# Performance work log

Hardware: AMD Instinct MI355X
Metric: run time of the kernel (lower is better)

## Reference

```python
import jax, jax.numpy as jnp
import numpy as np

B, T, IMG = 64, 20, 64
IN_DIM = IMG * IMG          # 4096, from x.view(B,-1,64*64)
C_IN = 8                    # input_channels
R_DIM = C_IN * 1024         # 8192, reshape(B,20,-1,32,32) constraint
NF = 64                     # num_filters
Z_DIM = 256
LIN_IN = 2 * NF * 7 * 7     # 6272


def setup_inputs() -> dict:
    key = jax.random.key(0)
    ks = jax.random.split(key, 10)
    x = jax.random.normal(ks[0], (B, T, IMG, IMG), jnp.float32)
    Win = jax.random.normal(ks[1], (IN_DIM, R_DIM), jnp.float32) / np.sqrt(IN_DIM).astype(np.float32)
    U = jax.random.normal(ks[2], (IN_DIM, R_DIM), jnp.float32) / np.sqrt(IN_DIM).astype(np.float32)
    Wr = jax.random.normal(ks[3], (R_DIM, R_DIM), jnp.float32) / np.sqrt(R_DIM).astype(np.float32)
    conv1_w = jax.random.normal(ks[4], (NF, C_IN, 3, 3, 3), jnp.float32) * 0.05
    conv1_b = jax.random.normal(ks[5], (NF,), jnp.float32) * 0.01
    conv2_w = jax.random.normal(ks[6], (2 * NF, NF, 3, 4, 4), jnp.float32) * 0.05
    conv2_b = jax.random.normal(ks[7], (2 * NF,), jnp.float32) * 0.01
    lin_w = jax.random.normal(ks[8], (Z_DIM, LIN_IN), jnp.float32) * 0.02
    lin_b = jax.random.normal(ks[9], (Z_DIM,), jnp.float32) * 0.01
    return {"x": x, "Win": Win, "U": U, "Wr": Wr,
            "conv1_w": conv1_w, "conv1_b": conv1_b,
            "conv2_w": conv2_w, "conv2_b": conv2_b,
            "lin_w": lin_w, "lin_b": lin_b}


def reference(x, Win, U, Wr, conv1_w, conv1_b, conv2_w, conv2_b, lin_w, lin_b):
    Bn = x.shape[0]
    xf = x.reshape(Bn, T, IN_DIM)                      # (B,T,4096)
    h0 = jnp.tanh(xf[:, 0] @ Win)                      # (B,R)
    xU = jnp.einsum('bti,ir->tbr', xf[:, 1:], U)       # precompute input drive (T-1,B,R)

    def step(h, xu):
        h = jnp.tanh(xu + h @ Wr)
        return h, h

    _, hs = jax.lax.scan(step, h0, xU)                 # (T-1,B,R)
    H = jnp.concatenate([h0[None], hs], axis=0)        # (T,B,R)
    H = jnp.swapaxes(H, 0, 1)                          # (B,T,R)

    h = H.reshape(Bn, T, C_IN, 32, 32).transpose(0, 2, 1, 3, 4)  # (B,C,T,32,32)
    dn = ('NCDHW', 'OIDHW', 'NCDHW')
    y = jax.lax.conv_general_dilated(h, conv1_w, (1, 2, 2),
                                     [(1, 1), (1, 1), (1, 1)], dimension_numbers=dn)
    y = y + conv1_b[None, :, None, None, None]
    y = jax.nn.leaky_relu(y, 0.01)                     # (B,NF,20,16,16)
    y = jax.lax.conv_general_dilated(y, conv2_w, (1, 2, 2),
                                     [(1, 1), (0, 0), (0, 0)], dimension_numbers=dn)
    y = y + conv2_b[None, :, None, None, None]
    y = jax.nn.leaky_relu(y, 0.01)                     # (B,2NF,20,7,7)

    y = y.reshape(Bn, -1, T, LIN_IN)                   # (B,1,20,6272), same row-major view as torch
    y = y @ lin_w.T + lin_b                            # (B,1,20,Z_DIM)
    mu, log_var = jnp.split(y, 2, axis=3)
    return mu, log_var
```

## Files before the change

kernel.cpp:

```cpp
#include <hip/hip_runtime.h>

typedef __bf16 v8bf __attribute__((ext_vector_type(8)));
typedef float  v4f  __attribute__((ext_vector_type(4)));
typedef unsigned short us8 __attribute__((ext_vector_type(8)));

__device__ __forceinline__ float bf2f(unsigned short u) {
    union { unsigned int i; float f; } v; v.i = ((unsigned int)u) << 16; return v.f;
}
__device__ __forceinline__ unsigned short f2bf(float f) {
    union { float f; unsigned int i; } v; v.f = f;
    return (unsigned short)((v.i + 0x7fffu + ((v.i >> 16) & 1u)) >> 16);
}
__device__ __forceinline__ int sw(int b) { return b ^ (((b >> 7) & 7) << 4); }

__global__ __launch_bounds__(256)
void transpose_f32_bf16(const float* __restrict__ src,
                        unsigned short* __restrict__ dst, int K, int N)
{
    __shared__ unsigned short tile[64][72];
    const int tid = threadIdx.x;
    const int c0 = blockIdx.x * 64, r0 = blockIdx.y * 64;
    const int tr = tid >> 2, tc4 = tid & 3;
    const float* sp = src + (size_t)(r0 + tr) * N + c0 + tc4 * 16;
#pragma unroll
    for (int j = 0; j < 4; ++j) {
        v4f f = *reinterpret_cast<const v4f*>(sp + j * 4);
#pragma unroll
        for (int e = 0; e < 4; ++e) tile[tr][tc4 * 16 + j * 4 + e] = f2bf(f[e]);
    }
    __syncthreads();
    const int ow = tid >> 3, och = tid & 7;
#pragma unroll
    for (int p = 0; p < 2; ++p) {
        int orow = p * 32 + ow;
        us8 o;
#pragma unroll
        for (int e = 0; e < 8; ++e) o[e] = tile[och * 8 + e][orow];
        *reinterpret_cast<us8*>(dst + (size_t)(c0 + orow) * K + r0 + och * 8) = o;
    }
}

__global__ __launch_bounds__(256)
void transpose_f32_bf16_tiled(const float* __restrict__ src,
                              unsigned short* __restrict__ dst, int N, int ktiles)
{
    __shared__ unsigned short tile[64][72];
    const int tid = threadIdx.x;
    const int c0 = blockIdx.x * 64, r0 = blockIdx.y * 64;
    const int tr = tid >> 2, tc4 = tid & 3;
    const float* sp = src + (size_t)(r0 + tr) * N + c0 + tc4 * 16;
#pragma unroll
    for (int j = 0; j < 4; ++j) {
        v4f f = *reinterpret_cast<const v4f*>(sp + j * 4);
#pragma unroll
        for (int e = 0; e < 4; ++e) tile[tr][tc4 * 16 + j * 4 + e] = f2bf(f[e]);
    }
    __syncthreads();
    const int ow = tid >> 3, och = tid & 7;
    unsigned short* tb = dst + ((size_t)blockIdx.x * ktiles + blockIdx.y) * 4096;
#pragma unroll
    for (int p = 0; p < 2; ++p) {
        int orow = p * 32 + ow;
        us8 o;
#pragma unroll
        for (int e = 0; e < 8; ++e) o[e] = tile[och * 8 + e][orow];
        *reinterpret_cast<us8*>(tb + orow * 64 + (och ^ (orow & 7)) * 8) = o;
    }
}

__global__ __launch_bounds__(256)
void cvt_x(const float* __restrict__ x, unsigned short* __restrict__ xb)
{
    int i = blockIdx.x * 256 + threadIdx.x;
    if (i >= 655360) return;
    v4f f0 = *reinterpret_cast<const v4f*>(x + (size_t)i * 8);
    v4f f1 = *reinterpret_cast<const v4f*>(x + (size_t)i * 8 + 4);
    us8 o;
#pragma unroll
    for (int e = 0; e < 4; ++e) { o[e] = f2bf(f0[e]); o[4 + e] = f2bf(f1[e]); }
    *reinterpret_cast<us8*>(xb + (size_t)i * 8) = o;
}

template<int BN, bool STORE_BF16, bool AF32, bool BF32, bool SWAPXY>
__global__ __launch_bounds__(256, 2)
void gemm_bt(const void* __restrict__ Ap, int lda_lo, int lda_hi,
             const void* __restrict__ BTp, int ldb,
             void* __restrict__ Cout, int ldc,
             int ksub, long long csplit_stride)
{
    constexpr int FN  = BN / 32;
    constexpr int BCH = BN / 32;
    const int tid = threadIdx.x;
    const int lane = tid & 63, wid = tid >> 6;
    const int wr = wid >> 1, wc = wid & 1;
    const int nt = SWAPXY ? blockIdx.y : blockIdx.x;
    const int mt = SWAPXY ? blockIdx.x : blockIdx.y;
    const int kz = blockIdx.z;
    const int n0 = nt * BN;
    const int kstart = kz * ksub;

    __shared__ unsigned short smem[(64 + BN) * 64];
    char* As = reinterpret_cast<char*>(smem);
    char* Bs = reinterpret_cast<char*>(smem + 64 * 64);

    const unsigned short* A16 = (const unsigned short*)Ap;
    const float*          A32 = (const float*)Ap;
    const unsigned short* B16 = (const unsigned short*)BTp;
    const float*          B32 = (const float*)BTp;

    const int arow = AF32 ? (tid >> 2) : (tid >> 3);
    const int aq   = AF32 ? (tid & 3) : (tid & 7);
    const float* Ab32 = A32 + (size_t)arow * lda_lo + (size_t)mt * lda_hi + kstart + aq * 16;
    const unsigned short* Ab16 = A16 + (size_t)arow * lda_lo + (size_t)mt * lda_hi + kstart + aq * 8;
    const int brow = tid >> 3, bq = tid & 7;
    const float* Bb32 = B32 + (size_t)(n0 + brow) * ldb + kstart + bq * 8;
    const unsigned short* Bb16 = B16 + (size_t)(n0 + brow) * ldb + kstart + bq * 8;

    v4f fa[4];
    us8 ra[2];
    v4f fb[BCH][2];
    us8 rb[BCH];

    auto load = [&](int kk) {
        if (AF32) {
#pragma unroll
            for (int j = 0; j < 4; ++j)
                fa[j] = *reinterpret_cast<const v4f*>(Ab32 + kk + j * 4);
        } else {
#pragma unroll
            for (int p = 0; p < 2; ++p)
                ra[p] = *reinterpret_cast<const us8*>(Ab16 + (size_t)(p * 32) * lda_lo + kk);
        }
        if (BF32) {
#pragma unroll
            for (int p = 0; p < BCH; ++p) {
                fb[p][0] = *reinterpret_cast<const v4f*>(Bb32 + (size_t)(p * 32) * ldb + kk);
                fb[p][1] = *reinterpret_cast<const v4f*>(Bb32 + (size_t)(p * 32) * ldb + kk + 4);
            }
        } else {
#pragma unroll
            for (int p = 0; p < BCH; ++p)
                rb[p] = *reinterpret_cast<const us8*>(Bb16 + (size_t)(p * 32) * ldb + kk);
        }
    };
    auto stage = [&]() {
        if (AF32) {
#pragma unroll
            for (int h = 0; h < 2; ++h) {
                us8 v;
#pragma unroll
                for (int e = 0; e < 8; ++e) v[e] = f2bf(fa[h * 2 + (e >> 2)][e & 3]);
                *reinterpret_cast<us8*>(As + arow * 128 + (((aq * 2 + h) * 16) ^ ((arow & 7) << 4))) = v;
            }
        } else {
#pragma unroll
            for (int p = 0; p < 2; ++p)
                *reinterpret_cast<us8*>(As + (arow + p * 32) * 128 + ((aq * 16) ^ ((arow & 7) << 4))) = ra[p];
        }
#pragma unroll
        for (int p = 0; p < BCH; ++p) {
            us8 v;
            if (BF32) {
#pragma unroll
                for (int e = 0; e < 8; ++e) v[e] = f2bf(fb[p][e >> 2][e & 3]);
            } else v = rb[p];
            *reinterpret_cast<us8*>(Bs + (brow + p * 32) * 128 + ((bq * 16) ^ ((brow & 7) << 4))) = v;
        }
    };

    v4f z4 = {0.f, 0.f, 0.f, 0.f};
    v4f acc[2][FN];
#pragma unroll
    for (int i = 0; i < 2; ++i)
#pragma unroll
        for (int j = 0; j < FN; ++j) acc[i][j] = z4;

    const int l15 = lane & 15, l4 = lane >> 4;
    const int nk = ksub / 64;
    load(0);
    for (int it = 0; it < nk; ++it) {
        __syncthreads();
        stage();
        __syncthreads();
        if (it + 1 < nk) load((it + 1) * 64);
#pragma unroll
        for (int ks = 0; ks < 2; ++ks) {
            const int kb = (ks * 32 + l4 * 8) * 2;
            v8bf af[2], bfr[FN];
#pragma unroll
            for (int fm = 0; fm < 2; ++fm) {
                int row = wr * 32 + fm * 16 + l15;
                af[fm] = *reinterpret_cast<const v8bf*>(As + row * 128 + (kb ^ ((row & 7) << 4)));
            }
#pragma unroll
            for (int fn = 0; fn < FN; ++fn) {
                int row = wc * (BN / 2) + fn * 16 + l15;
                bfr[fn] = *reinterpret_cast<const v8bf*>(Bs + row * 128 + (kb ^ ((row & 7) << 4)));
            }
#pragma unroll
            for (int fm = 0; fm < 2; ++fm)
#pragma unroll
                for (int fn = 0; fn < FN; ++fn)
                    acc[fm][fn] = __builtin_amdgcn_mfma_f32_16x16x32_bf16(af[fm], bfr[fn], acc[fm][fn], 0, 0, 0);
        }
    }
    const long long m0 = (long long)mt * 64;
#pragma unroll
    for (int fm = 0; fm < 2; ++fm)
#pragma unroll
        for (int fn = 0; fn < FN; ++fn)
#pragma unroll
            for (int r = 0; r < 4; ++r) {
                long long row = m0 + wr * 32 + fm * 16 + l4 * 4 + r;
                long long col = n0 + wc * (BN / 2) + fn * 16 + l15;
                long long idx = (long long)kz * csplit_stride + row * ldc + col;
                if (STORE_BF16) reinterpret_cast<unsigned short*>(Cout)[idx] = f2bf(acc[fm][fn][r]);
                else            reinterpret_cast<float*>(Cout)[idx]          = acc[fm][fn][r];
            }
}

#define KZ 4
__global__ __launch_bounds__(256, 2)
void scan_step(const unsigned short* __restrict__ A, int lda,
               const unsigned short* __restrict__ BTiles, int ktiles,
               int kper,
               const unsigned short* __restrict__ xu,
               unsigned short* __restrict__ hnext,
               unsigned short* __restrict__ Hbf, int t,
               float* __restrict__ part,
               unsigned int* __restrict__ tickets)
{
    const int tid = threadIdx.x, lane = tid & 63, wid = tid >> 6;
    const int wr = wid >> 1, wc = wid & 1;
    const int nt = blockIdx.x & 127, kz = blockIdx.x >> 7;
    const int n0 = nt * 64, kstart = kz * kper;
    const int l15 = lane & 15, l4 = lane >> 4;
    const int nit = kper >> 6;

    __shared__ unsigned short smem[32768];
    char* base = reinterpret_cast<char*>(smem);

    const int srow = tid >> 3, sq = tid & 7;
    const int gslot = sq ^ (srow & 7);
    const unsigned short* Asrc = A + (size_t)srow * lda + kstart + gslot * 8;
    const unsigned short* Bsrc = BTiles
        + ((size_t)(nt * ktiles + kz * (kper >> 6))) * 4096 + tid * 8;

    auto stage = [&](int buf, int it) {
        char* dA = base + buf * 16384 + wid * 1024;
        char* dB = dA + 8192;
        const int kk = it * 64;
#pragma unroll
        for (int p = 0; p < 2; ++p) {
            __builtin_amdgcn_global_load_lds(
                (const __attribute__((address_space(1))) void*)(Asrc + kk + (size_t)p * 32 * lda),
                (__attribute__((address_space(3))) void*)(dA + p * 4096), 16, 0, 0);
            __builtin_amdgcn_global_load_lds(
                (const __attribute__((address_space(1))) void*)(Bsrc + (size_t)it * 4096 + p * 2048),
                (__attribute__((address_space(3))) void*)(dB + p * 4096), 16, 0, 0);
        }
    };

    v4f acc00 = {0.f, 0.f, 0.f, 0.f};
    v4f acc01 = acc00, acc10 = acc00, acc11 = acc00;

    stage(0, 0); stage(1, 1); stage(2, 2);
    for (int it = 0; it < nit; ++it) {
        const int ahead = nit - 1 - it;
        if (ahead >= 2)      asm volatile("s_waitcnt vmcnt(8)" ::: "memory");
        else if (ahead == 1) asm volatile("s_waitcnt vmcnt(4)" ::: "memory");
        else                 asm volatile("s_waitcnt vmcnt(0)" ::: "memory");
        __builtin_amdgcn_s_barrier();
        __builtin_amdgcn_sched_barrier(0);
        if (it + 3 < nit) stage((it + 3) & 3, it + 3);
        const char* As = base + (it & 3) * 16384;
        const char* Bs = As + 8192;
#pragma unroll
        for (int ks = 0; ks < 2; ++ks) {
            const int kb = (ks * 32 + l4 * 8) * 2;
            v8bf a0, a1, b0, b1;
            { int row = wr * 32 + l15;      a0 = *reinterpret_cast<const v8bf*>(As + row * 128 + (kb ^ ((row & 7) << 4))); }
            { int row = wr * 32 + 16 + l15; a1 = *reinterpret_cast<const v8bf*>(As + row * 128 + (kb ^ ((row & 7) << 4))); }
            { int row = wc * 32 + l15;      b0 = *reinterpret_cast<const v8bf*>(Bs + row * 128 + (kb ^ ((row & 7) << 4))); }
            { int row = wc * 32 + 16 + l15; b1 = *reinterpret_cast<const v8bf*>(Bs + row * 128 + (kb ^ ((row & 7) << 4))); }
            acc00 = __builtin_amdgcn_mfma_f32_16x16x32_bf16(a0, b0, acc00, 0, 0, 0);
            acc01 = __builtin_amdgcn_mfma_f32_16x16x32_bf16(a0, b1, acc01, 0, 0, 0);
            acc10 = __builtin_amdgcn_mfma_f32_16x16x32_bf16(a1, b0, acc10, 0, 0, 0);
            acc11 = __builtin_amdgcn_mfma_f32_16x16x32_bf16(a1, b1, acc11, 0, 0, 0);
        }
    }

    float* mypart = part + (size_t)kz * 524288;
#pragma unroll
    for (int r = 0; r < 4; ++r) {
        int row0 = wr * 32 + l4 * 4 + r;
        int col0 = n0 + wc * 32 + l15;
        mypart[(size_t)row0 * 8192 + col0]             = acc00[r];
        mypart[(size_t)row0 * 8192 + col0 + 16]        = acc01[r];
        mypart[(size_t)(row0 + 16) * 8192 + col0]      = acc10[r];
        mypart[(size_t)(row0 + 16) * 8192 + col0 + 16] = acc11[r];
    }

    __shared__ int lastflag;
    __syncthreads();
    if (tid == 0) {
        unsigned int old = __hip_atomic_fetch_add(&tickets[nt], 1u,
                              __ATOMIC_ACQ_REL, __HIP_MEMORY_SCOPE_AGENT);
        lastflag = (old == KZ - 1);
    }
    __syncthreads();
    if (!lastflag) return;

    const int row = tid >> 2;
    const int c0 = n0 + (tid & 3) * 16;
    float pre[16];
    if (xu) {
        const us8* xp = reinterpret_cast<const us8*>(xu + (size_t)row * 8192 + c0);
        us8 x0 = xp[0], x1 = xp[1];
#pragma unroll
        for (int j = 0; j < 8; ++j) { pre[j] = bf2f(x0[j]); pre[8 + j] = bf2f(x1[j]); }
    } else {
#pragma unroll
        for (int j = 0; j < 16; ++j) pre[j] = 0.f;
    }
#pragma unroll
    for (int z = 0; z < KZ; ++z) {
        const float* pp = part + (size_t)z * 524288 + (size_t)row * 8192 + c0;
#pragma unroll
        for (int q = 0; q < 4; ++q) {
            v4f v = *reinterpret_cast<const v4f*>(pp + q * 4);
#pragma unroll
            for (int e = 0; e < 4; ++e) pre[q * 4 + e] += v[e];
        }
    }
    us8 o0, o1;
#pragma unroll
    for (int j = 0; j < 16; ++j) {
        unsigned short hb = f2bf(tanhf(pre[j]));
        if (j < 8) o0[j] = hb; else o1[j - 8] = hb;
        int col = c0 + j;
        Hbf[(((size_t)row * 20 + t) * 1024 + (col & 1023)) * 8 + (col >> 10)] = hb;
    }
    *reinterpret_cast<us8*>(hnext + (size_t)row * 8192 + c0)     = o0;
    *reinterpret_cast<us8*>(hnext + (size_t)row * 8192 + c0 + 8) = o1;
    if (tid == 0)
        __hip_atomic_store(&tickets[nt], 0u, __ATOMIC_RELAXED, __HIP_MEMORY_SCOPE_AGENT);
}

__global__ __launch_bounds__(256)
void cvt_w1(const float* __restrict__ w, unsigned short* __restrict__ o,
            unsigned int* __restrict__ tickets)
{
    if (blockIdx.x == 0 && threadIdx.x < 128) tickets[threadIdx.x] = 0;
    int idx = blockIdx.x * 256 + threadIdx.x;
    if (idx >= 64 * 224) return;
    int co = idx / 224, k = idx % 224;
    int g = k >> 3, ci = k & 7;
    float v = 0.f;
    if (g < 27) {
        int dt = g / 9, rr = g % 9, dy = rr / 3, dx = rr % 3;
        v = w[(((co * 8 + ci) * 3 + dt) * 3 + dy) * 3 + dx];
    }
    o[idx] = f2bf(v);
}
__global__ __launch_bounds__(256)
void cvt_w2(const float* __restrict__ w, unsigned short* __restrict__ o)
{
    int idx = blockIdx.x * 256 + threadIdx.x;
    if (idx >= 128 * 3072) return;
    int co = idx / 3072, k = idx % 3072;
    int g = k >> 6, ci = k & 63;
    int dt = g >> 4, dy = (g >> 2) & 3, dx = g & 3;
    o[idx] = f2bf(w[(((co * 64 + ci) * 3 + dt) * 4 + dy) * 4 + dx]);
}

__global__ __launch_bounds__(256, 2)
void conv1_kernel(const unsigned short* __restrict__ H,
                  const unsigned short* __restrict__ w1,
                  const float* __restrict__ bias,
                  unsigned short* __restrict__ y1)
{
    const int b = blockIdx.x, t = blockIdx.y;
    const int tid = threadIdx.x, lane = tid & 63, wid = tid >> 6;
    __shared__ unsigned short in_s[3 * 33 * 33 * 8];
    __shared__ unsigned short w_s[64 * 224];

    for (int i = tid; i < 13068; i += 256) reinterpret_cast<unsigned int*>(in_s)[i] = 0;
    __syncthreads();
    for (int idx = tid; idx < 3 * 1024; idx += 256) {
        int dt = idx >> 10, rem = idx & 1023;
        int iy = rem >> 5, ix = rem & 31;
        int ts = t + dt - 1;
        if (ts >= 0 && ts < 20) {
            us8 v = *reinterpret_cast<const us8*>(H + (((size_t)b * 20 + ts) * 1024 + rem) * 8);
            int byte = ((dt * 33 + iy + 1) * 33 + (ix + 1)) * 16;
            *reinterpret_cast<us8*>(reinterpret_cast<char*>(in_s) + sw(byte)) = v;
        }
    }
    for (int idx = tid; idx < 64 * 28; idx += 256) {
        int co = idx / 28, j = idx % 28;
        us8 v = *reinterpret_cast<const us8*>(w1 + co * 224 + j * 8);
        *reinterpret_cast<us8*>(reinterpret_cast<char*>(w_s) + sw(co * 448 + j * 16)) = v;
    }
    __syncthreads();

    const int l15 = lane & 15, l4 = lane >> 4;
    const int m_lo = wid * 64 + l15;
    v4f z4 = {0.f, 0.f, 0.f, 0.f};
    v4f acc[4][4];
#pragma unroll
    for (int i = 0; i < 4; ++i)
#pragma unroll
        for (int j = 0; j < 4; ++j) acc[i][j] = z4;

#pragma unroll
    for (int ks = 0; ks < 7; ++ks) {
        int g = ks * 4 + l4;
        int gc = g < 27 ? g : 26;
        int dt = gc / 9, rr = gc % 9, dy = rr / 3, dx = rr % 3;
        v8bf ap[4], aw[4];
#pragma unroll
        for (int fm = 0; fm < 4; ++fm) {
            int m = fm * 16 + m_lo;
            int py = m >> 4, px = m & 15;
            int byte = ((dt * 33 + 2 * py + dy) * 33 + 2 * px + dx) * 16;
            ap[fm] = *reinterpret_cast<const v8bf*>(reinterpret_cast<const char*>(in_s) + sw(byte));
        }
        int kb2 = (ks * 32 + l4 * 8) * 2;
#pragma unroll
        for (int fc = 0; fc < 4; ++fc) {
            int co = fc * 16 + l15;
            aw[fc] = *reinterpret_cast<const v8bf*>(reinterpret_cast<const char*>(w_s) + sw(co * 448 + kb2));
        }
#pragma unroll
        for (int fm = 0; fm < 4; ++fm)
#pragma unroll
            for (int fc = 0; fc < 4; ++fc)
                acc[fm][fc] = __builtin_amdgcn_mfma_f32_16x16x32_bf16(ap[fm], aw[fc], acc[fm][fc], 0, 0, 0);
    }
#pragma unroll
    for (int fm = 0; fm < 4; ++fm)
#pragma unroll
        for (int fc = 0; fc < 4; ++fc)
#pragma unroll
            for (int r = 0; r < 4; ++r) {
                int m  = wid * 64 + fm * 16 + l4 * 4 + r;
                int co = fc * 16 + l15;
                float v = acc[fm][fc][r] + bias[co];
                v = v > 0.f ? v : 0.01f * v;
                y1[(((size_t)b * 20 + t) * 256 + m) * 64 + co] = f2bf(v);
            }
}

__global__ __launch_bounds__(512, 2)
void conv2_kernel(const unsigned short* __restrict__ y1,
                  const unsigned short* __restrict__ w2,
                  const float* __restrict__ bias,
                  unsigned short* __restrict__ y2)
{
    const int b = blockIdx.x, t = blockIdx.y;
    const int tid = threadIdx.x, lane = tid & 63, wid = tid >> 6;
    const int wc = wid >> 1, wr = wid & 1;
    __shared__ unsigned short in_s[256 * 64];
    __shared__ unsigned short w_s[128 * 128];
    const int l15 = lane & 15, l4 = lane >> 4;

    const int m0v = wr * 32 + l15, m1v = m0v + 16;
    const int m0c = m0v < 49 ? m0v : 48, m1c = m1v < 49 ? m1v : 48;
    const int py0 = m0c / 7, px0 = m0c - py0 * 7;
    const int py1 = m1c / 7, px1 = m1c - py1 * 7;

    v4f acc[2][2];
#pragma unroll
    for (int i = 0; i < 2; ++i)
#pragma unroll
        for (int j = 0; j < 2; ++j) acc[i][j] = (v4f){0.f, 0.f, 0.f, 0.f};

    for (int dt = 0; dt < 3; ++dt) {
        int ts = t + dt - 1;
        __syncthreads();
        if (ts < 0 || ts >= 20) continue;
#pragma unroll
        for (int p = 0; p < 4; ++p) {
            int idx = tid + p * 512;
            int slot = idx >> 3, c8 = idx & 7;
            int yy = slot >> 4, xx = slot & 15;
            us8 v = *reinterpret_cast<const us8*>(y1 + (((size_t)b * 20 + ts) * 256 + slot) * 64 + c8 * 8);
            int cell = ((yy & 1) * 2 + (xx & 1)) * 64 + (yy >> 1) * 8 + (xx >> 1);
            int byte = cell * 128 + ((c8 * 16) ^ (((cell ^ (cell >> 3)) & 7) << 4));
            *reinterpret_cast<us8*>(reinterpret_cast<char*>(in_s) + byte) = v;
        }
        for (int kc = 0; kc < 8; ++kc) {
            __syncthreads();
#pragma unroll
            for (int p = 0; p < 4; ++p) {
                int idx = tid + p * 512;
                int co = idx >> 4, j = idx & 15;
                us8 v = *reinterpret_cast<const us8*>(w2 + (size_t)co * 3072 + dt * 1024 + kc * 128 + j * 8);
                *reinterpret_cast<us8*>(reinterpret_cast<char*>(w_s) + co * 256 + ((j * 16) ^ ((co & 7) << 4))) = v;
            }
            __syncthreads();
#pragma unroll
            for (int ks = 0; ks < 4; ++ks) {
                int klocal = ks * 32 + l4 * 8;
                int kk = kc * 128 + klocal;
                int dy = (kk >> 8) & 3, dx = (kk >> 6) & 3, ci0 = kk & 63;
                v8bf aw[2], bp[2];
#pragma unroll
                for (int fc = 0; fc < 2; ++fc) {
                    int co = wc * 32 + fc * 16 + l15;
                    aw[fc] = *reinterpret_cast<const v8bf*>(reinterpret_cast<const char*>(w_s)
                               + co * 256 + ((klocal * 2) ^ ((co & 7) << 4)));
                }
                int plane = ((dy & 1) << 1) | (dx & 1);
                int c0 = plane * 64 + (py0 + (dy >> 1)) * 8 + px0 + (dx >> 1);
                int c1 = plane * 64 + (py1 + (dy >> 1)) * 8 + px1 + (dx >> 1);
                bp[0] = *reinterpret_cast<const v8bf*>(reinterpret_cast<const char*>(in_s)
                          + c0 * 128 + ((ci0 * 2) ^ (((c0 ^ (c0 >> 3)) & 7) << 4)));
                bp[1] = *reinterpret_cast<const v8bf*>(reinterpret_cast<const char*>(in_s)
                          + c1 * 128 + ((ci0 * 2) ^ (((c1 ^ (c1 >> 3)) & 7) << 4)));
#pragma unroll
                for (int fc = 0; fc < 2; ++fc)
#pragma unroll
                    for (int fm = 0; fm < 2; ++fm)
                        acc[fc][fm] = __builtin_amdgcn_mfma_f32_16x16x32_bf16(aw[fc], bp[fm], acc[fc][fm], 0, 0, 0);
            }
        }
    }
#pragma unroll
    for (int fc = 0; fc < 2; ++fc)
#pragma unroll
        for (int fm = 0; fm < 2; ++fm)
#pragma unroll
            for (int r = 0; r < 4; ++r) {
                int co = wc * 32 + fc * 16 + l4 * 4 + r;
                int m  = wr * 32 + fm * 16 + l15;
                if (m < 49) {
                    float v = acc[fc][fm][r] + bias[co];
                    v = v > 0.f ? v : 0.01f * v;
                    y2[(((size_t)b * 128 + co) * 20 + t) * 49 + m] = f2bf(v);
                }
            }
}

__global__ __launch_bounds__(256)
void lin_epi(const float* __restrict__ linC, const float* __restrict__ lb,
             float* __restrict__ out)
{
    int i = blockIdx.x * 256 + threadIdx.x;
    int m = i >> 8, n = i & 255;
    float v = lb[n];
#pragma unroll
    for (int z = 0; z < 7; ++z) v += linC[(size_t)z * 327680 + i];
    size_t o = (n < 128) ? ((size_t)m * 128 + n) : (163840 + (size_t)m * 128 + (n - 128));
    out[o] = v;
}

extern "C" void kernel_launch(void* const* d_in, const int* in_sizes, int n_in,
                              void* d_out, int out_size, void* d_ws, size_t ws_size,
                              hipStream_t stream)
{
    const float* x   = (const float*)d_in[0];
    const float* Win = (const float*)d_in[1];
    const float* U   = (const float*)d_in[2];
    const float* Wr  = (const float*)d_in[3];
    const float* c1w = (const float*)d_in[4];
    const float* c1b = (const float*)d_in[5];
    const float* c2w = (const float*)d_in[6];
    const float* c2b = (const float*)d_in[7];
    const float* lw  = (const float*)d_in[8];
    const float* lb  = (const float*)d_in[9];

    char* ws = (char*)d_ws;
    unsigned short* WrTile = (unsigned short*)(ws);
    unsigned short* xbf  = (unsigned short*)(ws);
    unsigned short* WT   = (unsigned short*)(ws + 134217728ll);
    unsigned short* y1   = (unsigned short*)(ws + 134217728ll);
    unsigned short* y2   = (unsigned short*)(ws + 176160768ll);
    unsigned short* XALL = (unsigned short*)(ws + 201326592ll);
    unsigned short* Hbf  = (unsigned short*)(ws + 222298112ll);
    unsigned short* hb0  = (unsigned short*)(ws + 243269632ll);
    unsigned short* hb1  = (unsigned short*)(ws + 244318208ll);
    float*          part = (float*)        (ws + 245366784ll);
    float*          linC = (float*)        (ws + 245366784ll);
    unsigned short* w1bf = (unsigned short*)(ws + 254541824ll);
    unsigned short* w2bf = (unsigned short*)(ws + 254570496ll);
    unsigned int*   tick = (unsigned int*) (ws + 255356928ll);
    float*          out  = (float*)d_out;

    cvt_w1<<<56, 256, 0, stream>>>(c1w, w1bf, tick);
    cvt_w2<<<1536, 256, 0, stream>>>(c2w, w2bf);
    cvt_x<<<2560, 256, 0, stream>>>(x, xbf);

    transpose_f32_bf16_tiled<<<dim3(128, 64), 256, 0, stream>>>(Win, WT, 8192, 64);
    scan_step<<<512, 256, 0, stream>>>(xbf, 81920, WT, 64, 1024,
                                       (const unsigned short*)nullptr, hb0, Hbf, 0, part, tick);

    transpose_f32_bf16<<<dim3(128, 64), 256, 0, stream>>>(U, WT, 4096, 8192);
    gemm_bt<128, true, true, false, true><<<dim3(19, 64, 1), 256, 0, stream>>>(
        x + 4096, 81920, 4096, WT, 4096, XALL + 524288, 8192, 4096, 0ll);

    transpose_f32_bf16_tiled<<<dim3(128, 128), 256, 0, stream>>>(Wr, WrTile, 8192, 128);
    for (int t = 1; t < 20; ++t) {
        const unsigned short* hprev = (t & 1) ? hb0 : hb1;
        unsigned short*       hnext = (t & 1) ? hb1 : hb0;
        scan_step<<<512, 256, 0, stream>>>(hprev, 8192, WrTile, 128, 2048,
                                           XALL + (size_t)t * 524288, hnext, Hbf, t, part, tick);
    }

    conv1_kernel<<<dim3(64, 20), 256, 0, stream>>>(Hbf, w1bf, c1b, y1);
    conv2_kernel<<<dim3(64, 20), 512, 0, stream>>>(y1, w2bf, c2b, y2);

    gemm_bt<128, false, false, true, false><<<dim3(2, 20, 7), 256, 0, stream>>>(
        y2, 6272, 6272 * 64, lw, 6272, linC, 256, 896, 327680ll);
    lin_epi<<<1280, 256, 0, stream>>>(linC, lb, out);
}
```

Before: 1.549 ms.

## Add 8-way split-K scan step with 64x64 tiles and async LDS loads

New measurement: 1.811 ms. +16.9%, slower.

```diff
diff --git a/kernel.cpp b/kernel.cpp
--- a/kernel.cpp
+++ b/kernel.cpp
@@ -81,7 +81,7 @@
     *reinterpret_cast<us8*>(xb + (size_t)i * 8) = o;
 }
 
-template<int BN, bool STORE_BF16, bool AF32, bool BF32, bool SWAPXY>
+template<int BN, bool STORE_BF16, bool AF32, bool BF32>
 __global__ __launch_bounds__(256, 2)
 void gemm_bt(const void* __restrict__ Ap, int lda_lo, int lda_hi,
              const void* __restrict__ BTp, int ldb,
@@ -93,9 +93,7 @@
     const int tid = threadIdx.x;
     const int lane = tid & 63, wid = tid >> 6;
     const int wr = wid >> 1, wc = wid & 1;
-    const int nt = SWAPXY ? blockIdx.y : blockIdx.x;
-    const int mt = SWAPXY ? blockIdx.x : blockIdx.y;
-    const int kz = blockIdx.z;
+    const int nt = blockIdx.x, mt = blockIdx.y, kz = blockIdx.z;
     const int n0 = nt * BN;
     const int kstart = kz * ksub;
 
@@ -325,6 +323,134 @@
     }
 #pragma unroll
     for (int z = 0; z < KZ; ++z) {
+        const float* pp = part + (size_t)z * 524288 + (size_t)row * 8192 + c0;
+#pragma unroll
+        for (int q = 0; q < 4; ++q) {
+            v4f v = *reinterpret_cast<const v4f*>(pp + q * 4);
+#pragma unroll
+            for (int e = 0; e < 4; ++e) pre[q * 4 + e] += v[e];
+        }
+    }
+    us8 o0, o1;
+#pragma unroll
+    for (int j = 0; j < 16; ++j) {
+        unsigned short hb = f2bf(tanhf(pre[j]));
+        if (j < 8) o0[j] = hb; else o1[j - 8] = hb;
+        int col = c0 + j;
+        Hbf[(((size_t)row * 20 + t) * 1024 + (col & 1023)) * 8 + (col >> 10)] = hb;
+    }
+    *reinterpret_cast<us8*>(hnext + (size_t)row * 8192 + c0)     = o0;
+    *reinterpret_cast<us8*>(hnext + (size_t)row * 8192 + c0 + 8) = o1;
+    if (tid == 0)
+        __hip_atomic_store(&tickets[nt], 0u, __ATOMIC_RELAXED, __HIP_MEMORY_SCOPE_AGENT);
+}
+
+#define KZ2 8
+__global__ __launch_bounds__(256, 4)
+void scan_step2(const unsigned short* __restrict__ A, int lda,
+                const unsigned short* __restrict__ BTiles, int ktiles,
+                int kper,
+                const unsigned short* __restrict__ xu,
+                unsigned short* __restrict__ hnext,
+                unsigned short* __restrict__ Hbf, int t,
+                float* __restrict__ part,
+                unsigned int* __restrict__ tickets)
+{
+    const int tid = threadIdx.x, lane = tid & 63, wid = tid >> 6;
+    const int wr = wid >> 1, wc = wid & 1;
+    const int nt = blockIdx.x & 127, kz = blockIdx.x >> 7;
+    const int n0 = nt * 64, kstart = kz * kper;
+    const int l15 = lane & 15, l4 = lane >> 4;
+    const int nit = kper >> 6;
+
+    __shared__ unsigned short smem[16384];
+    char* base = reinterpret_cast<char*>(smem);
+
+    const int srow = tid >> 3, sq = tid & 7;
+    const int gslot = sq ^ (srow & 7);
+    const unsigned short* Asrc = A + (size_t)srow * lda + kstart + gslot * 8;
+    const unsigned short* Bsrc = BTiles
+        + ((size_t)(nt * ktiles + kz * (kper >> 6))) * 4096 + tid * 8;
+
+    auto stage = [&](int buf, int it) {
+        char* dA = base + buf * 16384 + wid * 1024;
+        char* dB = dA + 8192;
+        const int kk = it * 64;
+#pragma unroll
+        for (int p = 0; p < 2; ++p) {
+            __builtin_amdgcn_global_load_lds(
+                (const __attribute__((address_space(1))) void*)(Asrc + kk + (size_t)p * 32 * lda),
+                (__attribute__((address_space(3))) void*)(dA + p * 4096), 16, 0, 0);
+            __builtin_amdgcn_global_load_lds(
+                (const __attribute__((address_space(1))) void*)(Bsrc + (size_t)it * 4096 + p * 2048),
+                (__attribute__((address_space(3))) void*)(dB + p * 4096), 16, 0, 0);
+        }
+    };
+
+    v4f acc00 = {0.f, 0.f, 0.f, 0.f};
+    v4f acc01 = acc00, acc10 = acc00, acc11 = acc00;
+
+    stage(0, 0);
+    for (int it = 0; it < nit; ++it) {
+        const int cur = it & 1;
+        if (it + 1 < nit) {
+            stage(cur ^ 1, it + 1);
+            asm volatile("s_waitcnt vmcnt(4)" ::: "memory");
+        } else {
+            asm volatile("s_waitcnt vmcnt(0)" ::: "memory");
+        }
+        __builtin_amdgcn_s_barrier();
+        __builtin_amdgcn_sched_barrier(0);
+        const char* As = base + cur * 16384;
+        const char* Bs = As + 8192;
+#pragma unroll
+        for (int ks = 0; ks < 2; ++ks) {
+            const int kb = (ks * 32 + l4 * 8) * 2;
+            v8bf a0, a1, b0, b1;
+            { int row = wr * 32 + l15;      a0 = *reinterpret_cast<const v8bf*>(As + row * 128 + (kb ^ ((row & 7) << 4))); }
+            { int row = wr * 32 + 16 + l15; a1 = *reinterpret_cast<const v8bf*>(As + row * 128 + (kb ^ ((row & 7) << 4))); }
+            { int row = wc * 32 + l15;      b0 = *reinterpret_cast<const v8bf*>(Bs + row * 128 + (kb ^ ((row & 7) << 4))); }
+            { int row = wc * 32 + 16 + l15; b1 = *reinterpret_cast<const v8bf*>(Bs + row * 128 + (kb ^ ((row & 7) << 4))); }
+            acc00 = __builtin_amdgcn_mfma_f32_16x16x32_bf16(a0, b0, acc00, 0, 0, 0);
+            acc01 = __builtin_amdgcn_mfma_f32_16x16x32_bf16(a0, b1, acc01, 0, 0, 0);
+            acc10 = __builtin_amdgcn_mfma_f32_16x16x32_bf16(a1, b0, acc10, 0, 0, 0);
+            acc11 = __builtin_amdgcn_mfma_f32_16x16x32_bf16(a1, b1, acc11, 0, 0, 0);
+        }
+        __builtin_amdgcn_s_barrier();
+    }
+
+    float* mypart = part + (size_t)kz * 524288;
+#pragma unroll
+    for (int r = 0; r < 4; ++r) {
+        int row0 = wr * 32 + l4 * 4 + r;
+        int col0 = n0 + wc * 32 + l15;
+        mypart[(size_t)row0 * 8192 + col0]             = acc00[r];
+        mypart[(size_t)row0 * 8192 + col0 + 16]        = acc01[r];
+        mypart[(size_t)(row0 + 16) * 8192 + col0]      = acc10[r];
+        mypart[(size_t)(row0 + 16) * 8192 + col0 + 16] = acc11[r];
+    }
+
+    __shared__ int lastflag;
+    __syncthreads();
+    if (tid == 0) {
+        unsigned int old = __hip_atomic_fetch_add(&tickets[nt], 1u,
+                              __ATOMIC_ACQ_REL, __HIP_MEMORY_SCOPE_AGENT);
+        lastflag = (old == KZ2 - 1);
+    }
+    __syncthreads();
+    if (!lastflag) return;
+
+    const int row = tid >> 2;
+    const int c0 = n0 + (tid & 3) * 16;
+    float pre[16];
+    {
+        const us8* xp = reinterpret_cast<const us8*>(xu + (size_t)row * 8192 + c0);
+        us8 x0 = xp[0], x1 = xp[1];
+#pragma unroll
+        for (int j = 0; j < 8; ++j) { pre[j] = bf2f(x0[j]); pre[8 + j] = bf2f(x1[j]); }
+    }
+#pragma unroll
+    for (int z = 0; z < KZ2; ++z) {
         const float* pp = part + (size_t)z * 524288 + (size_t)row * 8192 + c0;
 #pragma unroll
         for (int q = 0; q < 4; ++q) {
@@ -575,6 +701,7 @@
     unsigned short* WrTile = (unsigned short*)(ws);
     unsigned short* xbf  = (unsigned short*)(ws);
     unsigned short* WT   = (unsigned short*)(ws + 134217728ll);
+    float*          part16 = (float*)      (ws + 134217728ll);
     unsigned short* y1   = (unsigned short*)(ws + 134217728ll);
     unsigned short* y2   = (unsigned short*)(ws + 176160768ll);
     unsigned short* XALL = (unsigned short*)(ws + 201326592ll);
@@ -597,21 +724,21 @@
                                        (const unsigned short*)nullptr, hb0, Hbf, 0, part, tick);
 
     transpose_f32_bf16<<<dim3(128, 64), 256, 0, stream>>>(U, WT, 4096, 8192);
-    gemm_bt<128, true, true, false, true><<<dim3(19, 64, 1), 256, 0, stream>>>(
+    gemm_bt<128, true, true, false><<<dim3(64, 19, 1), 256, 0, stream>>>(
         x + 4096, 81920, 4096, WT, 4096, XALL + 524288, 8192, 4096, 0ll);
 
     transpose_f32_bf16_tiled<<<dim3(128, 128), 256, 0, stream>>>(Wr, WrTile, 8192, 128);
     for (int t = 1; t < 20; ++t) {
         const unsigned short* hprev = (t & 1) ? hb0 : hb1;
         unsigned short*       hnext = (t & 1) ? hb1 : hb0;
-        scan_step<<<512, 256, 0, stream>>>(hprev, 8192, WrTile, 128, 2048,
-                                           XALL + (size_t)t * 524288, hnext, Hbf, t, part, tick);
+        scan_step2<<<1024, 256, 0, stream>>>(hprev, 8192, WrTile, 128, 1024,
+                                             XALL + (size_t)t * 524288, hnext, Hbf, t, part16, tick);
     }
 
     conv1_kernel<<<dim3(64, 20), 256, 0, stream>>>(Hbf, w1bf, c1b, y1);
     conv2_kernel<<<dim3(64, 20), 512, 0, stream>>>(y1, w2bf, c2b, y2);
 
-    gemm_bt<128, false, false, true, false><<<dim3(2, 20, 7), 256, 0, stream>>>(
+    gemm_bt<128, false, false, true><<<dim3(2, 20, 7), 256, 0, stream>>>(
         y2, 6272, 6272 * 64, lw, 6272, linC, 256, 896, 327680ll);
     lin_epi<<<1280, 256, 0, stream>>>(linC, lb, out);
 }
```
